# Kernel optimization log

Hardware: AMD Instinct MI355X
Metric: run time of the kernel (lower is better)

Reference implementation:

```python
import jax, jax.numpy as jnp
import numpy as np

CEP_ORDER = 24
ALPHA = 0.42
BETA = 0.2
ONSET = 2
IR_LENGTH = 128


def _freqt_matrix(in_order, out_order, alpha):
    # diffsptk FrequencyTransform precomputed matrix A (L2, L1): c2 = c1 @ A.T
    L1, L2 = in_order + 1, out_order + 1
    A = np.zeros((L2, L1), dtype=np.float64)
    A[0, :] = alpha ** np.arange(L1)
    if L2 > 1 and L1 > 1:
        A[1, 1:] = (alpha ** np.arange(L1 - 1, dtype=np.float64)) * np.arange(1, L1) * (1.0 - alpha * alpha)
    for i in range(2, L2):
        for j in range(1, L1):
            A[i, j] = A[i - 1, j - 1] + alpha * (A[i, j - 1] - A[i - 1, j])
    return A


def _mc2b_matrix(M, alpha):
    # b[m] = mc[m] - alpha*b[m+1]  =>  b[m] = sum_{j>=m} (-alpha)^(j-m) mc[j]
    j = np.arange(M + 1)
    P = j[None, :] - j[:, None]
    return np.where(P >= 0, (-alpha) ** np.maximum(P, 0), 0.0)


def _b2mc_matrix(M, alpha):
    # mc[m] = b[m] + alpha*b[m+1]
    return np.eye(M + 1) + alpha * np.eye(M + 1, k=1)


# constants derived from hyperparameters (buffers in the torch module)
A_FT = jnp.asarray(_freqt_matrix(CEP_ORDER, IR_LENGTH - 1, -ALPHA), dtype=jnp.float32)   # (128, 25)
A_MC2B = jnp.asarray(_mc2b_matrix(CEP_ORDER, ALPHA), dtype=jnp.float32)                  # (25, 25)
A_B2MC = jnp.asarray(_b2mc_matrix(CEP_ORDER, ALPHA), dtype=jnp.float32)                  # (25, 25)
_w = np.full(CEP_ORDER + 1, 1.0 + BETA, dtype=np.float32)
_w[:ONSET] = 1.0
WEIGHT = jnp.asarray(_w)                                                                  # (25,)


def _mc2en(mc):
    # mel-cepstrum -> energy: warp to linear cepstrum (len 128), power spectrum, r[0]
    c = jnp.einsum('...m,lm->...l', mc, A_FT)                 # (..., 128)
    spec = jnp.exp(2.0 * jnp.fft.rfft(c, n=IR_LENGTH).real)   # (..., 65), real power spectrum
    # r[0] of irfft(spec): DC + Nyquist once, interior bins twice (IR_LENGTH even)
    r0 = (spec[..., 0] + spec[..., -1] + 2.0 * jnp.sum(spec[..., 1:-1], axis=-1)) / IR_LENGTH
    return r0                                                  # (...,)


def setup_inputs() -> dict:
    key = jax.random.key(0)
    mc = 0.2 * jax.random.normal(key, (16, 32768, CEP_ORDER + 1), dtype=jnp.float32)
    return {"mc": mc}


def reference(mc):
    e1 = _mc2en(mc)                                            # energy before postfilter
    mc2 = mc * WEIGHT                                          # intensity-weighted cepstrum
    e2 = _mc2en(mc2)                                           # energy after weighting
    b2 = jnp.einsum('...m,nm->...n', mc2, A_MC2B)              # mc -> MLSA coefficients
    b2 = b2.at[..., 0].add(0.5 * jnp.log(e1 / e2))             # energy compensation on b[0]
    return jnp.einsum('...m,nm->...n', b2, A_B2MC)             # MLSA -> mel-cepstrum
```

## Files before the change

### kernel.cpp

```cpp
#include <hip/hip_runtime.h>


namespace cg {

constexpr int L  = 128;
constexpr int M1 = 25;

struct CosTab { double v[L]; };
constexpr CosTab make_costab() {
    CosTab t{};
    const double PI = 3.14159265358979323846;
    for (int i = 0; i < L; ++i) {
        int j = (i <= 64) ? i : i - 128;
        double x = (2.0 * PI * (double)j) / 128.0;
        double x2 = x * x, term = 1.0, s = 1.0;
        for (int n = 1; n <= 16; ++n) {
            term *= -x2 / ((2.0 * n - 1.0) * (2.0 * n));
            s += term;
        }
        t.v[i] = s;
    }
    return t;
}
constexpr CosTab CT = make_costab();

struct AMat { double v[L][M1]; };
constexpr AMat make_aft() {
    AMat A{};
    const double al = -0.42;
    double p = 1.0;
    for (int j = 0; j < M1; ++j) { A.v[0][j] = p; p *= al; }
    double q = 1.0;
    for (int j = 1; j < M1; ++j) { A.v[1][j] = q * (double)j * (1.0 - al * al); q *= al; }
    for (int i = 2; i < L; ++i)
        for (int j = 1; j < M1; ++j)
            A.v[i][j] = A.v[i - 1][j - 1] + al * (A.v[i][j - 1] - A.v[i - 1][j]);
    return A;
}
constexpr AMat AFT = make_aft();

struct Chunk { double v[8][M1]; };
template <int K0>
constexpr Chunk make_chunk() {
    Chunk c{};
    for (int kk = 0; kk < 8; ++kk) {
        int k = K0 + kk;
        for (int m = 0; m < M1; ++m) {
            double s = 0.0;
            for (int l = 0; l < L; ++l)
                s += AFT.v[l][m] * CT.v[(k * l) & 127];
            c.v[kk][m] = s;
        }
    }
    return c;
}
constexpr Chunk CH0 = make_chunk<0>();
constexpr Chunk CH1 = make_chunk<8>();
constexpr Chunk CH2 = make_chunk<16>();
constexpr Chunk CH3 = make_chunk<24>();
constexpr Chunk CH4 = make_chunk<32>();
constexpr Chunk CH5 = make_chunk<40>();
constexpr Chunk CH6 = make_chunk<48>();
constexpr Chunk CH7 = make_chunk<56>();
constexpr Chunk CH8 = make_chunk<64>();

constexpr double chunkval(int bin, int m) {
    const Chunk* chs[9] = { &CH0, &CH1, &CH2, &CH3, &CH4, &CH5, &CH6, &CH7, &CH8 };
    return chs[bin >> 3]->v[bin & 7][m];
}

constexpr double blogical(int k, int col) {
    const double LOG2E = 1.44269504088896340736;
    if (col >= 130) return (k == 25) ? -1.0e4 : 0.0;
    int bin = (col < 65) ? col : (col - 65);
    if (k == 25) return (bin == 0 || bin == 64) ? 0.0 : 1.0;
    if (k > 25) return 0.0;
    double c = LOG2E * 2.0 * chunkval(bin, k);
    if (col >= 65 && k >= 2) c *= 1.2;
    return c;
}

constexpr unsigned short f2h(double v) {
    if (v == 0.0) return 0;
    unsigned short s = 0;
    if (v < 0) { s = 0x8000; v = -v; }
    int e = 0;
    while (v >= 2.0) { v *= 0.5; ++e; }
    while (v < 1.0)  { v *= 2.0; --e; }
    if (e > 15) return (unsigned short)(s | 0x7c00);
    if (e < -14) return s;
    int mant = (int)((v - 1.0) * 1024.0 + 0.5);
    if (mant == 1024) { mant = 0; ++e; if (e > 15) return (unsigned short)(s | 0x7c00); }
    return (unsigned short)(s | ((e + 15) << 10) | mant);
}

struct Tile { unsigned short v[64][8]; };
template <int N>
constexpr Tile make_tile() {
    Tile t{};
    for (int l = 0; l < 64; ++l)
        for (int j = 0; j < 8; ++j)
            t.v[l][j] = f2h(blogical((l >> 4) * 8 + j, N * 16 + (l & 15)));
    return t;
}
constexpr Tile T0 = make_tile<0>();
constexpr Tile T1 = make_tile<1>();
constexpr Tile T2 = make_tile<2>();
constexpr Tile T3 = make_tile<3>();
constexpr Tile T4 = make_tile<4>();
constexpr Tile T5 = make_tile<5>();
constexpr Tile T6 = make_tile<6>();
constexpr Tile T7 = make_tile<7>();
constexpr Tile T8 = make_tile<8>();

struct BH { alignas(16) unsigned short v[9][64][8]; };
constexpr BH make_bh() {
    BH b{};
    const Tile* ts[9] = { &T0, &T1, &T2, &T3, &T4, &T5, &T6, &T7, &T8 };
    for (int n = 0; n < 9; ++n)
        for (int l = 0; l < 64; ++l)
            for (int j = 0; j < 8; ++j)
                b.v[n][l][j] = ts[n]->v[l][j];
    return b;
}

}

__device__ const cg::BH g_Bh = cg::make_bh();

typedef _Float16 f16x8 __attribute__((ext_vector_type(8)));
typedef float    f32x4 __attribute__((ext_vector_type(4)));

__global__ __launch_bounds__(256, 6)
void mcpf_kernel(const float* __restrict__ mc, float* __restrict__ out) {
    __shared__ __align__(16) float sbuf[4 * 1600 + 16];
    const int tid  = threadIdx.x;
    const int lane = tid & 63;
    const int wv   = tid >> 6;
    const int r0   = lane & 15;
    const int kg   = lane >> 4;

    float* __restrict__ wbuf = &sbuf[wv * 1600];
    const long long base4 = (long long)blockIdx.x * 1600 + wv * 400;

    f16x8 bfrag[9];
#pragma unroll
    for (int n = 0; n < 9; ++n)
        bfrag[n] = *reinterpret_cast<const f16x8*>(&g_Bh.v[n][lane][0]);

    const float4* __restrict__ src4 =
        reinterpret_cast<const float4*>(mc) + base4;
#pragma unroll
    for (int j = 0; j < 7; ++j) {
        int idx = lane + j * 64;
        if (idx < 400) {
            __builtin_amdgcn_global_load_lds(
                (const __attribute__((address_space(1))) float*)(const float*)(src4 + idx),
                (__attribute__((address_space(3))) float*)(wbuf + j * 256),
                16, 0, 0);
        }
    }
    asm volatile("s_waitcnt vmcnt(0)" ::: "memory");

    float4* __restrict__ wb4  = reinterpret_cast<float4*>(wbuf);
    float4* __restrict__ dst4 = reinterpret_cast<float4*>(out) + base4;

#pragma unroll
    for (int g = 0; g < 4; ++g) {
        const float* __restrict__ arow = &wbuf[(g * 16 + r0) * 25 + kg * 8];

        float tmp[8];
#pragma unroll
        for (int j = 0; j < 8; ++j) tmp[j] = arow[j];
        f16x8 af;
        af[0] = (_Float16)tmp[0];
        af[1] = (kg == 3) ? (_Float16)1.0f : (_Float16)tmp[1];
#pragma unroll
        for (int j = 2; j < 8; ++j)
            af[j] = (kg == 3) ? (_Float16)0.0f : (_Float16)tmp[j];

        float s1 = 0.0f, s2 = 0.0f;
#pragma unroll
        for (int n = 0; n < 9; ++n) {
            f32x4 acc = {0.f, 0.f, 0.f, 0.f};
            acc = __builtin_amdgcn_mfma_f32_16x16x32_f16(bfrag[n], af, acc, 0, 0, 0);
            float e0 = __builtin_amdgcn_exp2f(acc[0]);
            float e1 = __builtin_amdgcn_exp2f(acc[1]);
            float e2 = __builtin_amdgcn_exp2f(acc[2]);
            float e3 = __builtin_amdgcn_exp2f(acc[3]);
            if (n < 4) {
                s1 += (e0 + e1) + (e2 + e3);
            } else if (n == 4) {
                float h = (e0 + e1) + (e2 + e3);
                bool c = (kg == 0);
                s1 += c ? e0 : 0.0f;
                s2 += c ? (h - e0) : h;
            } else {
                s2 += (e0 + e1) + (e2 + e3);
            }
        }

        s1 += __shfl_xor(s1, 16);
        s1 += __shfl_xor(s1, 32);
        s2 += __shfl_xor(s2, 16);
        s2 += __shfl_xor(s2, 32);

        const float d = 0.34657359027997264f *
                        (__builtin_amdgcn_logf(s1) - __builtin_amdgcn_logf(s2));

#pragma unroll
        for (int j = 0; j < 2; ++j) {
            int t = lane + j * 64;
            if (t < 100) {
                int idx = g * 100 + t;
                float4 v = wb4[idx];
                int f = idx * 4;
                int q = f / 25;
                int r = f - 25 * q;
                int srcl = ((r == 0) ? q : q + 1) & 15;
                float dv = __shfl(d, srcl);
                v.x *= (r     < 2)                  ? 1.0f : 1.2f;
                v.y *= (r + 1 < 2 || r + 1 == 25)   ? 1.0f : 1.2f;
                v.z *= (r + 2 == 25 || r + 2 == 26) ? 1.0f : 1.2f;
                v.w *= (r + 3 == 25 || r + 3 == 26) ? 1.0f : 1.2f;
                if (r == 0)  v.x += dv;
                if (r == 22) v.w += dv;
                if (r == 23) v.z += dv;
                if (r == 24) v.y += dv;
                dst4[idx] = v;
            }
        }
    }
}

extern "C" void kernel_launch(void* const* d_in, const int* in_sizes, int n_in,
                              void* d_out, int out_size, void* d_ws, size_t ws_size,
                              hipStream_t stream) {
    const float* mc = (const float*)d_in[0];
    float* out = (float*)d_out;
    const int rows = in_sizes[0] / 25;
    const int blocks = rows / 256;
    mcpf_kernel<<<dim3(blocks), dim3(256), 0, stream>>>(mc, out);
}
```

Measured before the change: 24.69 us.

## Double-buffer per-wave LDS staging to overlap global loads with MFMA compute

Each wave now handles 128 rows in four 32-row stages instead of 64 rows at once. The next stage's global-to-LDS async load is issued into a second buffer while the current one is computed, and partial vmcnt waits are used so load latency is hidden behind MFMA, exp and store work. The grid is halved and the occupancy hint lowered from 6 to 4 blocks per CU. In exchange there are fewer waves in flight, and the vmcnt counts are hand-tuned, which depends on how many load and store instructions each wave actually issues.

```diff
diff --git a/kernel.cpp b/kernel.cpp
--- a/kernel.cpp
+++ b/kernel.cpp
@@ -131,106 +131,127 @@
 typedef _Float16 f16x8 __attribute__((ext_vector_type(8)));
 typedef float    f32x4 __attribute__((ext_vector_type(4)));
 
-__global__ __launch_bounds__(256, 6)
+__global__ __launch_bounds__(256, 4)
 void mcpf_kernel(const float* __restrict__ mc, float* __restrict__ out) {
-    __shared__ __align__(16) float sbuf[4 * 1600 + 16];
+    __shared__ __align__(16) float sbuf[4 * 1600 + 8];
     const int tid  = threadIdx.x;
     const int lane = tid & 63;
     const int wv   = tid >> 6;
     const int r0   = lane & 15;
     const int kg   = lane >> 4;
 
-    float* __restrict__ wbuf = &sbuf[wv * 1600];
-    const long long base4 = (long long)blockIdx.x * 1600 + wv * 400;
+    float* __restrict__ wbase = &sbuf[wv * 1600];
+    const long long gw = (long long)blockIdx.x * 4 + wv;
+    const long long t0f4 = gw * 800;
+
+    const float4* __restrict__ src4  = reinterpret_cast<const float4*>(mc);
+    float4*       __restrict__ dst4g = reinterpret_cast<float4*>(out);
 
     f16x8 bfrag[9];
 #pragma unroll
     for (int n = 0; n < 9; ++n)
         bfrag[n] = *reinterpret_cast<const f16x8*>(&g_Bh.v[n][lane][0]);
 
-    const float4* __restrict__ src4 =
-        reinterpret_cast<const float4*>(mc) + base4;
-#pragma unroll
-    for (int j = 0; j < 7; ++j) {
-        int idx = lane + j * 64;
-        if (idx < 400) {
-            __builtin_amdgcn_global_load_lds(
-                (const __attribute__((address_space(1))) float*)(const float*)(src4 + idx),
-                (__attribute__((address_space(3))) float*)(wbuf + j * 256),
-                16, 0, 0);
-        }
-    }
-    asm volatile("s_waitcnt vmcnt(0)" ::: "memory");
-
-    float4* __restrict__ wb4  = reinterpret_cast<float4*>(wbuf);
-    float4* __restrict__ dst4 = reinterpret_cast<float4*>(out) + base4;
-
-#pragma unroll
-    for (int g = 0; g < 4; ++g) {
-        const float* __restrict__ arow = &wbuf[(g * 16 + r0) * 25 + kg * 8];
-
-        float tmp[8];
-#pragma unroll
-        for (int j = 0; j < 8; ++j) tmp[j] = arow[j];
-        f16x8 af;
-        af[0] = (_Float16)tmp[0];
-        af[1] = (kg == 3) ? (_Float16)1.0f : (_Float16)tmp[1];
-#pragma unroll
-        for (int j = 2; j < 8; ++j)
-            af[j] = (kg == 3) ? (_Float16)0.0f : (_Float16)tmp[j];
-
-        float s1 = 0.0f, s2 = 0.0f;
-#pragma unroll
-        for (int n = 0; n < 9; ++n) {
-            f32x4 acc = {0.f, 0.f, 0.f, 0.f};
-            acc = __builtin_amdgcn_mfma_f32_16x16x32_f16(bfrag[n], af, acc, 0, 0, 0);
-            float e0 = __builtin_amdgcn_exp2f(acc[0]);
-            float e1 = __builtin_amdgcn_exp2f(acc[1]);
-            float e2 = __builtin_amdgcn_exp2f(acc[2]);
-            float e3 = __builtin_amdgcn_exp2f(acc[3]);
-            if (n < 4) {
-                s1 += (e0 + e1) + (e2 + e3);
-            } else if (n == 4) {
-                float h = (e0 + e1) + (e2 + e3);
-                bool c = (kg == 0);
-                s1 += c ? e0 : 0.0f;
-                s2 += c ? (h - e0) : h;
-            } else {
-                s2 += (e0 + e1) + (e2 + e3);
+#define STAGE(b, t)                                                          \
+    do {                                                                     \
+        const float4* __restrict__ s_ = src4 + t0f4 + (t) * 200;             \
+        float* db_ = wbase + (b) * 800;                                      \
+        _Pragma("unroll")                                                    \
+        for (int j_ = 0; j_ < 3; ++j_)                                       \
+            __builtin_amdgcn_global_load_lds(                                \
+                (const __attribute__((address_space(1))) float*)             \
+                    (const float*)(s_ + lane + j_ * 64),                     \
+                (__attribute__((address_space(3))) float*)(db_ + j_ * 256),  \
+                16, 0, 0);                                                   \
+        if (lane < 8)                                                        \
+            __builtin_amdgcn_global_load_lds(                                \
+                (const __attribute__((address_space(1))) float*)             \
+                    (const float*)(s_ + lane + 192),                         \
+                (__attribute__((address_space(3))) float*)(db_ + 768),       \
+                16, 0, 0);                                                   \
+    } while (0)
+
+    STAGE(0, 0);
+
+#pragma unroll
+    for (int t = 0; t < 4; ++t) {
+        if (t < 3) STAGE((t + 1) & 1, t + 1);
+
+        if (t == 0 || t == 3) asm volatile("s_waitcnt vmcnt(4)" ::: "memory");
+        else                  asm volatile("s_waitcnt vmcnt(8)" ::: "memory");
+
+        float* __restrict__ cbuf = wbase + (t & 1) * 800;
+        float4* __restrict__ cb4 = reinterpret_cast<float4*>(cbuf);
+        float4* __restrict__ dt4 = dst4g + t0f4 + t * 200;
+
+#pragma unroll
+        for (int g = 0; g < 2; ++g) {
+            const float* __restrict__ arow = &cbuf[(g * 16 + r0) * 25 + kg * 8];
+
+            float tmp[8];
+#pragma unroll
+            for (int j = 0; j < 8; ++j) tmp[j] = arow[j];
+            f16x8 af;
+            af[0] = (_Float16)tmp[0];
+            af[1] = (kg == 3) ? (_Float16)1.0f : (_Float16)tmp[1];
+#pragma unroll
+            for (int j = 2; j < 8; ++j)
+                af[j] = (kg == 3) ? (_Float16)0.0f : (_Float16)tmp[j];
+
+            float s1 = 0.0f, s2 = 0.0f;
+#pragma unroll
+            for (int n = 0; n < 9; ++n) {
+                f32x4 acc = {0.f, 0.f, 0.f, 0.f};
+                acc = __builtin_amdgcn_mfma_f32_16x16x32_f16(bfrag[n], af, acc, 0, 0, 0);
+                float e0 = __builtin_amdgcn_exp2f(acc[0]);
+                float e1 = __builtin_amdgcn_exp2f(acc[1]);
+                float e2 = __builtin_amdgcn_exp2f(acc[2]);
+                float e3 = __builtin_amdgcn_exp2f(acc[3]);
+                if (n < 4) {
+                    s1 += (e0 + e1) + (e2 + e3);
+                } else if (n == 4) {
+                    float h = (e0 + e1) + (e2 + e3);
+                    bool c = (kg == 0);
+                    s1 += c ? e0 : 0.0f;
+                    s2 += c ? (h - e0) : h;
+                } else {
+                    s2 += (e0 + e1) + (e2 + e3);
+                }
             }
-        }
-
-        s1 += __shfl_xor(s1, 16);
-        s1 += __shfl_xor(s1, 32);
-        s2 += __shfl_xor(s2, 16);
-        s2 += __shfl_xor(s2, 32);
-
-        const float d = 0.34657359027997264f *
-                        (__builtin_amdgcn_logf(s1) - __builtin_amdgcn_logf(s2));
-
-#pragma unroll
-        for (int j = 0; j < 2; ++j) {
-            int t = lane + j * 64;
-            if (t < 100) {
-                int idx = g * 100 + t;
-                float4 v = wb4[idx];
-                int f = idx * 4;
-                int q = f / 25;
-                int r = f - 25 * q;
-                int srcl = ((r == 0) ? q : q + 1) & 15;
-                float dv = __shfl(d, srcl);
-                v.x *= (r     < 2)                  ? 1.0f : 1.2f;
-                v.y *= (r + 1 < 2 || r + 1 == 25)   ? 1.0f : 1.2f;
-                v.z *= (r + 2 == 25 || r + 2 == 26) ? 1.0f : 1.2f;
-                v.w *= (r + 3 == 25 || r + 3 == 26) ? 1.0f : 1.2f;
-                if (r == 0)  v.x += dv;
-                if (r == 22) v.w += dv;
-                if (r == 23) v.z += dv;
-                if (r == 24) v.y += dv;
-                dst4[idx] = v;
+
+            s1 += __shfl_xor(s1, 16);
+            s1 += __shfl_xor(s1, 32);
+            s2 += __shfl_xor(s2, 16);
+            s2 += __shfl_xor(s2, 32);
+
+            const float d = 0.34657359027997264f *
+                            (__builtin_amdgcn_logf(s1) - __builtin_amdgcn_logf(s2));
+
+#pragma unroll
+            for (int j = 0; j < 2; ++j) {
+                int t2 = lane + j * 64;
+                if (t2 < 100) {
+                    int idx = g * 100 + t2;
+                    float4 v = cb4[idx];
+                    int f = idx * 4;
+                    int q = f / 25;
+                    int r = f - 25 * q;
+                    int srcl = ((r == 0) ? q : q + 1) & 15;
+                    float dv = __shfl(d, srcl);
+                    v.x *= (r     < 2)                  ? 1.0f : 1.2f;
+                    v.y *= (r + 1 < 2 || r + 1 == 25)   ? 1.0f : 1.2f;
+                    v.z *= (r + 2 == 25 || r + 2 == 26) ? 1.0f : 1.2f;
+                    v.w *= (r + 3 == 25 || r + 3 == 26) ? 1.0f : 1.2f;
+                    if (r == 0)  v.x += dv;
+                    if (r == 22) v.w += dv;
+                    if (r == 23) v.z += dv;
+                    if (r == 24) v.y += dv;
+                    dt4[idx] = v;
+                }
             }
         }
     }
+#undef STAGE
 }
 
 extern "C" void kernel_launch(void* const* d_in, const int* in_sizes, int n_in,
@@ -239,6 +260,6 @@
     const float* mc = (const float*)d_in[0];
     float* out = (float*)d_out;
     const int rows = in_sizes[0] / 25;
-    const int blocks = rows / 256;
+    const int blocks = rows / 512;
     mcpf_kernel<<<dim3(blocks), dim3(256), 0, stream>>>(mc, out);
 }
```

Measured after the change: 24.28 us, median of 2. About the same (-1.7%).
